# Optimization experiments

Measured on AMD Instinct MI355X. Metric: run time of the kernel, lower is better.

Reference implementation:

```python
import jax, jax.numpy as jnp
import numpy as np

TRAJ_LEN = 25      # save points, as in the original module
N_SUB = 8          # fixed Tsit5 substeps per save interval (replaces adaptive PID stepping)
BATCH = 524288

# Tsit5 Butcher tableau (Tsitouras 2011), same method diffrax.Tsit5 uses.
A21 = 0.161
A31, A32 = -0.008480655492356989, 0.335480655492357
A41, A42, A43 = 2.8971530571054935, -6.359448489975075, 4.3622954328695815
A51, A52, A53, A54 = 5.325864828439257, -11.748883564062828, 7.4955393428898365, -0.09249506636175525
A61, A62, A63, A64, A65 = 5.86145544294642, -12.92096931784711, 8.159367898576159, -0.071584973281401, -0.028269050394068383
# 5th-order solution weights (b == a7j, FSAL)
B1, B2, B3, B4, B5, B6 = 0.09646076681806523, 0.01, 0.4798896504144996, 1.379008574103742, -3.290069515436081, 2.324710524099774


def setup_inputs() -> dict:
    key = jax.random.key(0)
    k1, k2 = jax.random.split(key)
    x0s = jax.random.normal(k1, (BATCH, 2), dtype=jnp.float32)
    matrix = 0.1 * jax.random.normal(k2, (2, 2), dtype=jnp.float32)
    T = jnp.float32(2.0)
    return {"x0s": x0s, "matrix": matrix, "T": T}


def reference(x0s, matrix, T):
    # dx/dt = T * (matrix @ x); integrate on t in [0,1], save at 25 equispaced times.
    h = jnp.float32(1.0 / ((TRAJ_LEN - 1) * N_SUB))

    def f(y):  # batched vector field: [B,2] @ [2,2]^T
        return T * (y @ matrix.T)

    def tsit5_step(y):
        k1 = f(y)
        k2 = f(y + h * (A21 * k1))
        k3 = f(y + h * (A31 * k1 + A32 * k2))
        k4 = f(y + h * (A41 * k1 + A42 * k2 + A43 * k3))
        k5 = f(y + h * (A51 * k1 + A52 * k2 + A53 * k3 + A54 * k4))
        k6 = f(y + h * (A61 * k1 + A62 * k2 + A63 * k3 + A64 * k4 + A65 * k5))
        return y + h * (B1 * k1 + B2 * k2 + B3 * k3 + B4 * k4 + B5 * k5 + B6 * k6)

    def interval(y, _):
        def sub(yy, __):
            return tsit5_step(yy), None
        y, _ = jax.lax.scan(sub, y, None, length=N_SUB)
        return y, y

    _, ys = jax.lax.scan(interval, x0s, None, length=TRAJ_LEN - 1)  # [24,B,2]
    trajs = jnp.concatenate([x0s[:, None, :], jnp.moveaxis(ys, 0, 1)], axis=1)  # [B,25,2]
    num_steps = jnp.int32(x0s.shape[0] * (TRAJ_LEN - 1) * N_SUB)  # total steps analog of sum(num_steps)
    return trajs, num_steps
```

## Files before the change

### kernel.cpp

```cpp
#include <hip/hip_runtime.h>

#define TRAJ_LEN 25
#define N_SUB 8

typedef float fx4 __attribute__((ext_vector_type(4)));

#define CA21 0.161
#define CA31 -0.008480655492356989
#define CA32 0.335480655492357
#define CA41 2.8971530571054935
#define CA42 -6.359448489975075
#define CA43 4.3622954328695815
#define CA51 5.325864828439257
#define CA52 -11.748883564062828
#define CA53 7.4955393428898365
#define CA54 -0.09249506636175525
#define CA61 5.86145544294642
#define CA62 -12.92096931784711
#define CA63 8.159367898576159
#define CA64 -0.071584973281401
#define CA65 -0.028269050394068383
#define CB1 0.09646076681806523
#define CB2 0.01
#define CB3 0.4798896504144996
#define CB4 1.379008574103742
#define CB5 -3.290069515436081
#define CB6 2.324710524099774

struct M2 { double a, b, c, d; };

__device__ __forceinline__ M2 mmul(const M2& x, const M2& y) {
    return { x.a * y.a + x.b * y.c, x.a * y.b + x.b * y.d,
             x.c * y.a + x.d * y.c, x.c * y.b + x.d * y.d };
}
__device__ __forceinline__ M2 msc(double s, const M2& x) {
    return { s * x.a, s * x.b, s * x.c, s * x.d };
}
__device__ __forceinline__ M2 madd(const M2& x, const M2& y) {
    return { x.a + y.a, x.b + y.b, x.c + y.c, x.d + y.d };
}
__device__ __forceinline__ M2 eyeph(double h, const M2& x) {
    return { 1.0 + h * x.a, h * x.b, h * x.c, 1.0 + h * x.d };
}

__global__ void setup_kernel(const float* __restrict__ mat,
                             const float* __restrict__ Tp,
                             float4* __restrict__ gpow,
                             float* __restrict__ out, int out_last,
                             float nsteps) {
    const int lane = threadIdx.x;
    const double T = (double)Tp[0];
    const double h = (double)(float)(1.0 / ((TRAJ_LEN - 1) * N_SUB));
    const M2 A = { T * (double)mat[0], T * (double)mat[1],
                   T * (double)mat[2], T * (double)mat[3] };

    M2 S1 = A;
    M2 S2 = mmul(A, eyeph(h, msc(CA21, S1)));
    M2 S3 = mmul(A, eyeph(h, madd(msc(CA31, S1), msc(CA32, S2))));
    M2 S4 = mmul(A, eyeph(h, madd(madd(msc(CA41, S1), msc(CA42, S2)), msc(CA43, S3))));
    M2 S5 = mmul(A, eyeph(h, madd(madd(madd(msc(CA51, S1), msc(CA52, S2)), msc(CA53, S3)), msc(CA54, S4))));
    M2 S6 = mmul(A, eyeph(h, madd(madd(madd(madd(msc(CA61, S1), msc(CA62, S2)), msc(CA63, S3)), msc(CA64, S4)), msc(CA65, S5))));
    M2 S = eyeph(h, madd(madd(madd(madd(madd(msc(CB1, S1), msc(CB2, S2)), msc(CB3, S3)), msc(CB4, S4)), msc(CB5, S5)), msc(CB6, S6)));
    M2 G2 = mmul(S, S);
    M2 G4 = mmul(G2, G2);
    M2 G  = mmul(G4, G4);

    if (lane < TRAJ_LEN) {
        M2 P = { 1.0, 0.0, 0.0, 1.0 };
        M2 Q = G;
        int n = lane;
        #pragma unroll
        for (int b = 0; b < 5; ++b) {
            if (n & 1) P = mmul(Q, P);
            n >>= 1;
            Q = mmul(Q, Q);
        }
        gpow[lane] = make_float4((float)P.a, (float)P.b, (float)P.c, (float)P.d);
        if (lane == 0) out[out_last] = nsteps;
    }
}

__global__ __launch_bounds__(256) void traj_kernel(
        const float2* __restrict__ x0,
        const float4* __restrict__ gpow,
        fx4* __restrict__ out, int n4) {
    __shared__ float4 g[TRAJ_LEN];
    if (threadIdx.x < TRAJ_LEN) g[threadIdx.x] = gpow[threadIdx.x];
    __syncthreads();

    const int t = blockIdx.x * 256 + threadIdx.x;
    if (t >= n4) return;

    const int o0 = 2 * t;
    const int e0 = o0 / TRAJ_LEN;
    const int i0 = o0 - e0 * TRAJ_LEN;
    int e1 = e0, i1 = i0 + 1;
    if (i1 == TRAJ_LEN) { i1 = 0; e1 = e0 + 1; }

    const float2 p0 = x0[e0];
    const float2 p1 = x0[e1];
    const float4 g0 = g[i0];
    const float4 g1 = g[i1];

    fx4 r;
    r.x = fmaf(g0.x, p0.x, g0.y * p0.y);
    r.y = fmaf(g0.z, p0.x, g0.w * p0.y);
    r.z = fmaf(g1.x, p1.x, g1.y * p1.y);
    r.w = fmaf(g1.z, p1.x, g1.w * p1.y);

    __builtin_nontemporal_store(r, &out[t]);
}

extern "C" void kernel_launch(void* const* d_in, const int* in_sizes, int n_in,
                              void* d_out, int out_size, void* d_ws, size_t ws_size,
                              hipStream_t stream) {
    const float* x0s = (const float*)d_in[0];
    const float* mat = (const float*)d_in[1];
    const float* T   = (const float*)d_in[2];
    float* out = (float*)d_out;
    float4* gpow = (float4*)d_ws;

    const int batch = in_sizes[0] / 2;
    const long long nsteps = (long long)batch * (TRAJ_LEN - 1) * N_SUB;

    const int traj_floats = batch * TRAJ_LEN * 2;
    const int n4 = traj_floats / 4;
    const int blocks = (n4 + 255) / 256;

    hipLaunchKernelGGL(setup_kernel, dim3(1), dim3(64), 0, stream,
                       mat, T, gpow, out, out_size - 1, (float)nsteps);
    hipLaunchKernelGGL(traj_kernel, dim3(blocks), dim3(256), 0, stream,
                       (const float2*)x0s, (const float4*)gpow,
                       (fx4*)out, n4);
}
```

Before: 130.5 us.

## Fuse setup into trajectory kernel with per-block matrix powers and grid-stride loop

```diff
diff --git a/kernel.cpp b/kernel.cpp
--- a/kernel.cpp
+++ b/kernel.cpp
@@ -43,72 +43,75 @@
     return { 1.0 + h * x.a, h * x.b, h * x.c, 1.0 + h * x.d };
 }
 
-__global__ void setup_kernel(const float* __restrict__ mat,
-                             const float* __restrict__ Tp,
-                             float4* __restrict__ gpow,
-                             float* __restrict__ out, int out_last,
-                             float nsteps) {
-    const int lane = threadIdx.x;
-    const double T = (double)Tp[0];
-    const double h = (double)(float)(1.0 / ((TRAJ_LEN - 1) * N_SUB));
-    const M2 A = { T * (double)mat[0], T * (double)mat[1],
-                   T * (double)mat[2], T * (double)mat[3] };
+__global__ __launch_bounds__(256) void fused_kernel(
+        const float2* __restrict__ x0,
+        const float* __restrict__ mat,
+        const float* __restrict__ Tp,
+        fx4* __restrict__ out, float* __restrict__ out_scalar,
+        int n4, int out_last, float nsteps,
+        int de, int di) {
+    __shared__ float4 g[TRAJ_LEN];
 
-    M2 S1 = A;
-    M2 S2 = mmul(A, eyeph(h, msc(CA21, S1)));
-    M2 S3 = mmul(A, eyeph(h, madd(msc(CA31, S1), msc(CA32, S2))));
-    M2 S4 = mmul(A, eyeph(h, madd(madd(msc(CA41, S1), msc(CA42, S2)), msc(CA43, S3))));
-    M2 S5 = mmul(A, eyeph(h, madd(madd(madd(msc(CA51, S1), msc(CA52, S2)), msc(CA53, S3)), msc(CA54, S4))));
-    M2 S6 = mmul(A, eyeph(h, madd(madd(madd(madd(msc(CA61, S1), msc(CA62, S2)), msc(CA63, S3)), msc(CA64, S4)), msc(CA65, S5))));
-    M2 S = eyeph(h, madd(madd(madd(madd(madd(msc(CB1, S1), msc(CB2, S2)), msc(CB3, S3)), msc(CB4, S4)), msc(CB5, S5)), msc(CB6, S6)));
-    M2 G2 = mmul(S, S);
-    M2 G4 = mmul(G2, G2);
-    M2 G  = mmul(G4, G4);
+    if (threadIdx.x < 64) {
+        const double T = (double)Tp[0];
+        const double h = (double)(float)(1.0 / ((TRAJ_LEN - 1) * N_SUB));
+        const M2 A = { T * (double)mat[0], T * (double)mat[1],
+                       T * (double)mat[2], T * (double)mat[3] };
 
-    if (lane < TRAJ_LEN) {
-        M2 P = { 1.0, 0.0, 0.0, 1.0 };
-        M2 Q = G;
-        int n = lane;
-        #pragma unroll
-        for (int b = 0; b < 5; ++b) {
-            if (n & 1) P = mmul(Q, P);
-            n >>= 1;
-            Q = mmul(Q, Q);
+        M2 S1 = A;
+        M2 S2 = mmul(A, eyeph(h, msc(CA21, S1)));
+        M2 S3 = mmul(A, eyeph(h, madd(msc(CA31, S1), msc(CA32, S2))));
+        M2 S4 = mmul(A, eyeph(h, madd(madd(msc(CA41, S1), msc(CA42, S2)), msc(CA43, S3))));
+        M2 S5 = mmul(A, eyeph(h, madd(madd(madd(msc(CA51, S1), msc(CA52, S2)), msc(CA53, S3)), msc(CA54, S4))));
+        M2 S6 = mmul(A, eyeph(h, madd(madd(madd(madd(msc(CA61, S1), msc(CA62, S2)), msc(CA63, S3)), msc(CA64, S4)), msc(CA65, S5))));
+        M2 S = eyeph(h, madd(madd(madd(madd(madd(msc(CB1, S1), msc(CB2, S2)), msc(CB3, S3)), msc(CB4, S4)), msc(CB5, S5)), msc(CB6, S6)));
+        M2 G2 = mmul(S, S);
+        M2 G4 = mmul(G2, G2);
+        M2 G  = mmul(G4, G4);
+
+        const int lane = threadIdx.x;
+        if (lane < TRAJ_LEN) {
+            M2 P = { 1.0, 0.0, 0.0, 1.0 };
+            M2 Q = G;
+            int n = lane;
+            #pragma unroll
+            for (int b = 0; b < 5; ++b) {
+                if (n & 1) P = mmul(Q, P);
+                n >>= 1;
+                Q = mmul(Q, Q);
+            }
+            g[lane] = make_float4((float)P.a, (float)P.b, (float)P.c, (float)P.d);
         }
-        gpow[lane] = make_float4((float)P.a, (float)P.b, (float)P.c, (float)P.d);
-        if (lane == 0) out[out_last] = nsteps;
+        if (lane == 0 && blockIdx.x == 0) out_scalar[out_last] = nsteps;
     }
-}
-
-__global__ __launch_bounds__(256) void traj_kernel(
-        const float2* __restrict__ x0,
-        const float4* __restrict__ gpow,
-        fx4* __restrict__ out, int n4) {
-    __shared__ float4 g[TRAJ_LEN];
-    if (threadIdx.x < TRAJ_LEN) g[threadIdx.x] = gpow[threadIdx.x];
     __syncthreads();
 
-    const int t = blockIdx.x * 256 + threadIdx.x;
-    if (t >= n4) return;
+    const int stride = gridDim.x * 256;
+    const int t0 = blockIdx.x * 256 + threadIdx.x;
 
-    const int o0 = 2 * t;
-    const int e0 = o0 / TRAJ_LEN;
-    const int i0 = o0 - e0 * TRAJ_LEN;
-    int e1 = e0, i1 = i0 + 1;
-    if (i1 == TRAJ_LEN) { i1 = 0; e1 = e0 + 1; }
+    int e0 = (2 * t0) / TRAJ_LEN;
+    int i0 = 2 * t0 - e0 * TRAJ_LEN;
 
-    const float2 p0 = x0[e0];
-    const float2 p1 = x0[e1];
-    const float4 g0 = g[i0];
-    const float4 g1 = g[i1];
+    for (int t = t0; t < n4; t += stride) {
+        int i1 = i0 + 1, e1 = e0;
+        if (i1 == TRAJ_LEN) { i1 = 0; e1 = e0 + 1; }
 
-    fx4 r;
-    r.x = fmaf(g0.x, p0.x, g0.y * p0.y);
-    r.y = fmaf(g0.z, p0.x, g0.w * p0.y);
-    r.z = fmaf(g1.x, p1.x, g1.y * p1.y);
-    r.w = fmaf(g1.z, p1.x, g1.w * p1.y);
+        const float2 p0 = x0[e0];
+        const float2 p1 = x0[e1];
+        const float4 g0 = g[i0];
+        const float4 g1 = g[i1];
 
-    __builtin_nontemporal_store(r, &out[t]);
+        fx4 r;
+        r.x = fmaf(g0.x, p0.x, g0.y * p0.y);
+        r.y = fmaf(g0.z, p0.x, g0.w * p0.y);
+        r.z = fmaf(g1.x, p1.x, g1.y * p1.y);
+        r.w = fmaf(g1.z, p1.x, g1.w * p1.y);
+
+        __builtin_nontemporal_store(r, &out[t]);
+
+        e0 += de; i0 += di;
+        if (i0 >= TRAJ_LEN) { i0 -= TRAJ_LEN; e0 += 1; }
+    }
 }
 
 extern "C" void kernel_launch(void* const* d_in, const int* in_sizes, int n_in,
@@ -118,18 +121,20 @@
     const float* mat = (const float*)d_in[1];
     const float* T   = (const float*)d_in[2];
     float* out = (float*)d_out;
-    float4* gpow = (float4*)d_ws;
 
     const int batch = in_sizes[0] / 2;
     const long long nsteps = (long long)batch * (TRAJ_LEN - 1) * N_SUB;
 
     const int traj_floats = batch * TRAJ_LEN * 2;
     const int n4 = traj_floats / 4;
-    const int blocks = (n4 + 255) / 256;
 
-    hipLaunchKernelGGL(setup_kernel, dim3(1), dim3(64), 0, stream,
-                       mat, T, gpow, out, out_size - 1, (float)nsteps);
-    hipLaunchKernelGGL(traj_kernel, dim3(blocks), dim3(256), 0, stream,
-                       (const float2*)x0s, (const float4*)gpow,
-                       (fx4*)out, n4);
+    const int blocks = 2048;
+    const int stride = blocks * 256;
+    const int de = (2 * stride) / TRAJ_LEN;
+    const int di = (2 * stride) % TRAJ_LEN;
+
+    hipLaunchKernelGGL(fused_kernel, dim3(blocks), dim3(256), 0, stream,
+                       (const float2*)x0s, mat, T,
+                       (fx4*)out, out, n4, out_size - 1, (float)nsteps,
+                       de, di);
 }
```

Measured after the change: 123.4 us. -5.5%, faster.
